# Kernel optimization log

Measured on AMD Instinct MI355X. Metric: run time of the kernel, lower is better.

## Reference

```python
import jax, jax.numpy as jnp
import numpy as np
from jax import lax

B, T, IN, H, OUT = 64, 512, 256, 1024, 512

def _uniform(key, shape, std):
    return jax.random.uniform(key, shape, jnp.float32, -std, std)

def setup_inputs() -> dict:
    key = jax.random.key(0)
    ks = jax.random.split(key, 12)
    std = 1.0 / np.sqrt(H)
    return {
        "x": jax.random.normal(ks[0], (B, T, IN), jnp.float32),
        "Wx0": _uniform(ks[1], (H, IN), std), "bx0": _uniform(ks[2], (H,), std),
        "Wh0": _uniform(ks[3], (H, H), std),  "bh0": _uniform(ks[4], (H,), std),
        "Wx1": _uniform(ks[5], (H, H), std),  "bx1": _uniform(ks[6], (H,), std),
        "Wh1": _uniform(ks[7], (H, H), std),  "bh1": _uniform(ks[8], (H,), std),
        "Wfc": _uniform(ks[9], (OUT, H), 1.0 / np.sqrt(H)),
        "bfc": _uniform(ks[10], (OUT,), 1.0 / np.sqrt(H)),
    }

def _run_layer(xs, Wx, bx, Wh, bh):
    # xs: [B, T, D_in] -> hidden sequence [B, T, H]
    xproj = jnp.einsum('btd,hd->bth', xs, Wx) + bx + bh  # precompute input projection
    def step(h, xp):
        h = jnp.tanh(xp + h @ Wh.T)
        return h, h
    h0 = jnp.zeros((xs.shape[0], Wh.shape[0]), xs.dtype)
    _, hs = lax.scan(step, h0, jnp.swapaxes(xproj, 0, 1))  # [T, B, H]
    return jnp.swapaxes(hs, 0, 1)

def reference(x, Wx0, bx0, Wh0, bh0, Wx1, bx1, Wh1, bh1, Wfc, bfc):
    h1 = _run_layer(x, Wx0, bx0, Wh0, bh0)   # layer 0 hidden sequence
    h2 = _run_layer(h1, Wx1, bx1, Wh1, bh1)  # layer 1 hidden sequence
    last = h2[:, -1, :]                       # last timestep of top layer
    return last @ Wfc.T + bfc
```

## Files before the change

### kernel.cpp

```cpp
#include <hip/hip_runtime.h>
#include <hip/hip_bf16.h>

#define Bb   64
#define Tt   512
#define INN  256
#define HH   1024
#define OUTN 512

#define NCOL 32
#define MG   16
#define NGRP (Bb / MG)
#define NSLOT 64
#define FSTR 8

typedef __attribute__((ext_vector_type(8))) short bf16x8;
typedef __attribute__((ext_vector_type(4))) float f32x4;

__device__ __forceinline__ unsigned short f2b(float f) {
  unsigned u = __float_as_uint(f);
  u += 0x7FFFu + ((u >> 16) & 1u);
  return (unsigned short)(u >> 16);
}
__device__ __forceinline__ float b2f(unsigned short u) {
  return __uint_as_float((unsigned)u << 16);
}

__device__ __forceinline__ unsigned int cohLoadU32(const unsigned int* p) {
  return __hip_atomic_load(p, __ATOMIC_RELAXED, __HIP_MEMORY_SCOPE_AGENT);
}
__device__ __forceinline__ unsigned long long cohLoadU64(const unsigned long long* p) {
  return __hip_atomic_load(p, __ATOMIC_RELAXED, __HIP_MEMORY_SCOPE_AGENT);
}
__device__ __forceinline__ unsigned short cohLoadU16(const unsigned short* p) {
  return __hip_atomic_load(p, __ATOMIC_RELAXED, __HIP_MEMORY_SCOPE_AGENT);
}
__device__ __forceinline__ void cohStoreU16(unsigned short* p, unsigned short v) {
  __hip_atomic_store(p, v, __ATOMIC_RELAXED, __HIP_MEMORY_SCOPE_AGENT);
}
__device__ __forceinline__ void cohStoreU32(unsigned int* p, unsigned int v) {
  __hip_atomic_store(p, v, __ATOMIC_RELAXED, __HIP_MEMORY_SCOPE_AGENT);
}

__device__ __forceinline__ void aload(bf16x8& d, const short* p) {
  asm volatile("global_load_dwordx4 %0, %1, off sc0 sc1" : "=v"(d) : "v"(p));
}
#define VMW(N)                                                   \
  do {                                                           \
    asm volatile("s_waitcnt vmcnt(" #N ")" ::: "memory");        \
    __builtin_amdgcn_sched_barrier(0);                           \
  } while (0)

__device__ __forceinline__ f32x4 splat4(float v) { f32x4 r = {v, v, v, v}; return r; }

union U16 { unsigned long long u[2]; bf16x8 v; };

__global__ void cvt4(const float* __restrict__ in, unsigned short* __restrict__ out, int n4) {
  int i = blockIdx.x * blockDim.x + threadIdx.x;
  if (i >= n4) return;
  float4 v = ((const float4*)in)[i];
  ushort4 o;
  o.x = f2b(v.x); o.y = f2b(v.y); o.z = f2b(v.z); o.w = f2b(v.w);
  ((ushort4*)out)[i] = o;
}

__global__ void addv(const float* __restrict__ a, const float* __restrict__ b,
                     float* __restrict__ o, int n) {
  int i = blockIdx.x * blockDim.x + threadIdx.x;
  if (i < n) o[i] = a[i] + b[i];
}

__global__ void zerok(unsigned int* __restrict__ p, int n) {
  int i = blockIdx.x * blockDim.x + threadIdx.x;
  if (i < n) p[i] = 0u;
}

__device__ __forceinline__ void waitflags(const unsigned int* gf, int l, unsigned need) {
#pragma clang loop unroll(disable)
  for (int guard = 0; guard < 4000000; ++guard) {
    unsigned f = cohLoadU32(gf + l * FSTR);
    if (__all((int)(f >= need))) return;
  }
}

__device__ __forceinline__ f32x4 comp8(const bf16x8* ab, const short* Wrow,
                                       int rx, int lh, int kk0, f32x4 acc) {
#pragma unroll
  for (int i = 0; i < 8; ++i) {
    const int s = (((kk0 + i) << 2) + lh) ^ rx;
    bf16x8 w = *(const bf16x8*)(Wrow + (s << 3));
    acc = __builtin_amdgcn_mfma_f32_16x16x32_bf16(ab[i], w, acc, 0, 0, 0);
  }
  return acc;
}

__device__ __forceinline__ f32x4 kphase(const short* Ap, const short* Wrow,
                                        int rx, int lh, f32x4 acc) {
  f32x4 acc2 = {0, 0, 0, 0};
  bf16x8 a0[8], a1[8];
#pragma unroll
  for (int i = 0; i < 8; ++i) aload(a0[i], Ap + i * 32);
#pragma unroll
  for (int i = 0; i < 8; ++i) aload(a1[i], Ap + 256 + i * 32);
  VMW(8);
  acc = comp8(a0, Wrow, rx, lh, 0, acc);
#pragma unroll
  for (int i = 0; i < 8; ++i) aload(a0[i], Ap + 512 + i * 32);
  VMW(8);
  acc2 = comp8(a1, Wrow, rx, lh, 8, acc2);
#pragma unroll
  for (int i = 0; i < 8; ++i) aload(a1[i], Ap + 768 + i * 32);
  VMW(8);
  acc = comp8(a0, Wrow, rx, lh, 16, acc);
  VMW(0);
  acc2 = comp8(a1, Wrow, rx, lh, 24, acc2);
  return acc + acc2;
}

__global__ __launch_bounds__(128) void rnn3(
    const __hip_bfloat16* __restrict__ xs,
    const __hip_bfloat16* __restrict__ Wx0, const __hip_bfloat16* __restrict__ Wh0,
    const __hip_bfloat16* __restrict__ Wx1, const __hip_bfloat16* __restrict__ Wh1,
    const float* __restrict__ b0s, const float* __restrict__ b1s,
    __hip_bfloat16* __restrict__ P0, __hip_bfloat16* __restrict__ P1,
    unsigned int* flags)
{
  __shared__ short Wl[NCOL * HH];
  const int tid = threadIdx.x;
  const int l   = tid & 63;
  const int wv  = tid >> 6;
  const int bid = blockIdx.x;
  const int stage = bid % 3;
  const int idx = bid / 3;
  const int j   = idx & 31;
  const int g   = idx >> 5;
  const int n0  = j * NCOL;
  const int rowA = g * MG;
  const int fr = l & 15;
  const int lh = l >> 4;
  const int rb = lh << 2;
  const int ccol = n0 + wv * 16 + fr;
  const int rx = (wv * 16 + fr) & 7;

  const short* Wg = (const short*)(stage == 0 ? Wh0 : (stage == 1 ? Wx1 : Wh1));
  for (int i = tid; i < NCOL * 128; i += 128) {
    const int r = i >> 7, p = i & 127, gs = p ^ (r & 7);
    *(bf16x8*)(Wl + r * HH + p * 8) = *(const bf16x8*)(Wg + (long)(n0 + r) * HH + gs * 8);
  }
  __syncthreads();
  const short* Wrow = Wl + (wv * 16 + fr) * HH;

  unsigned int* gf0 = flags + (0 * NGRP + g) * (NSLOT * FSTR);
  unsigned int* gfx = flags + (1 * NGRP + g) * (NSLOT * FSTR);
  unsigned int* gf1 = flags + (2 * NGRP + g) * (NSLOT * FSTR);
  const int wslot = (j * 2 + wv) * FSTR;
  const long laneA = (long)(rowA + fr) * HH + (lh << 3);
  unsigned short* P0u = (unsigned short*)P0;
  unsigned short* P1u = (unsigned short*)P1;

  if (stage == 0) {
    const float bias = b0s[ccol];
    const short* xrow = (const short*)xs + (long)(rowA + fr) * (Tt * INN) + (lh << 3);
    const short* Wx0row = (const short*)Wx0 + (long)ccol * INN + (lh << 3);
    bf16x8 wx[8];
#pragma unroll
    for (int c = 0; c < 8; ++c) wx[c] = *(const bf16x8*)(Wx0row + c * 32);
    f32x4 acc = splat4(bias);
#pragma unroll
    for (int c = 0; c < 8; ++c) {
      bf16x8 a = *(const bf16x8*)(xrow + c * 32);
      acc = __builtin_amdgcn_mfma_f32_16x16x32_bf16(a, wx[c], acc, 0, 0, 0);
    }
    for (int t = 0; t < Tt; ++t) {
      if (t > 0) {
        waitflags(gf0, l, (unsigned)t);
        acc = kphase((const short*)P0 + (long)(t - 1) * (Bb * HH) + laneA, Wrow, rx, lh, acc);
      }
      const long cb = ((long)t * Bb + rowA + rb) * HH + ccol;
#pragma unroll
      for (int r = 0; r < 4; ++r) cohStoreU16(P0u + cb + (long)r * HH, f2b(tanhf(acc[r])));
      asm volatile("s_waitcnt vmcnt(0)" ::: "memory");
      if (l == 0) cohStoreU32(gf0 + wslot, (unsigned)(t + 1));
      if (t + 1 < Tt) {
        acc = splat4(bias);
        const short* xr = xrow + (t + 1) * INN;
#pragma unroll
        for (int c = 0; c < 8; ++c) {
          bf16x8 a = *(const bf16x8*)(xr + c * 32);
          acc = __builtin_amdgcn_mfma_f32_16x16x32_bf16(a, wx[c], acc, 0, 0, 0);
        }
      }
    }
  } else if (stage == 1) {
    const float bias = b1s[ccol];
    for (int t = 0; t < Tt; ++t) {
      waitflags(gf0, l, (unsigned)(t + 1));
      f32x4 acc = kphase((const short*)P0 + (long)t * (Bb * HH) + laneA, Wrow, rx, lh,
                         splat4(bias));
      const long cb = ((long)t * Bb + rowA + rb) * HH + ccol;
#pragma unroll
      for (int r = 0; r < 4; ++r) cohStoreU16(P1u + cb + (long)r * HH, f2b(acc[r]));
      asm volatile("s_waitcnt vmcnt(0)" ::: "memory");
      if (l == 0) cohStoreU32(gfx + wslot, (unsigned)(t + 1));
    }
  } else {
    for (int t = 0; t < Tt; ++t) {
      waitflags(gfx, l, (unsigned)(t + 1));
      const long cb = ((long)t * Bb + rowA + rb) * HH + ccol;
      float xb[4];
#pragma unroll
      for (int r = 0; r < 4; ++r)
        xb[r] = b2f(cohLoadU16(P1u + cb + (long)r * HH));
      f32x4 acc = {0, 0, 0, 0};
      if (t > 0) {
        waitflags(gf1, l, (unsigned)t);
        acc = kphase((const short*)P1 + (long)(t - 1) * (Bb * HH) + laneA, Wrow, rx, lh, acc);
      }
#pragma unroll
      for (int r = 0; r < 4; ++r)
        cohStoreU16(P1u + cb + (long)r * HH, f2b(tanhf(acc[r] + xb[r])));
      asm volatile("s_waitcnt vmcnt(0)" ::: "memory");
      if (l == 0) cohStoreU32(gf1 + wslot, (unsigned)(t + 1));
    }
  }
}

__global__ void fc_kernel(const __hip_bfloat16* __restrict__ A,
                          const __hip_bfloat16* __restrict__ W,
                          const float* __restrict__ bias,
                          float* __restrict__ C)
{
  const int l   = threadIdx.x;
  const int m0  = blockIdx.x << 4;
  const int n0  = blockIdx.y << 6;
  const int r16 = l & 15;
  const int lh  = l >> 4;

  const unsigned long long* Au =
      (const unsigned long long*)((const short*)A + (long)(m0 + r16) * HH);
  const short* Wp = (const short*)W;
  const long w0 = (long)(n0 + r16) * HH + (lh << 3);
  const long wS = (long)HH << 4;

  f32x4 acc0 = {0,0,0,0}, acc1 = {0,0,0,0}, acc2 = {0,0,0,0}, acc3 = {0,0,0,0};
  for (int kc = 0; kc < HH; kc += 32) {
    U16 a;
    a.u[0] = cohLoadU64(Au + (kc >> 2) + (lh << 1));
    a.u[1] = cohLoadU64(Au + (kc >> 2) + (lh << 1) + 1);
    bf16x8 b0 = *(const bf16x8*)(Wp + w0 +          kc);
    bf16x8 b1 = *(const bf16x8*)(Wp + w0 + wS     + kc);
    bf16x8 b2 = *(const bf16x8*)(Wp + w0 + 2 * wS + kc);
    bf16x8 b3 = *(const bf16x8*)(Wp + w0 + 3 * wS + kc);
    acc0 = __builtin_amdgcn_mfma_f32_16x16x32_bf16(a.v, b0, acc0, 0, 0, 0);
    acc1 = __builtin_amdgcn_mfma_f32_16x16x32_bf16(a.v, b1, acc1, 0, 0, 0);
    acc2 = __builtin_amdgcn_mfma_f32_16x16x32_bf16(a.v, b2, acc2, 0, 0, 0);
    acc3 = __builtin_amdgcn_mfma_f32_16x16x32_bf16(a.v, b3, acc3, 0, 0, 0);
  }
  const int col = l & 15;
  const int rbb = (l >> 4) << 2;
#define FCEP(FIDX, ACC)                                                       \
  { const int n = n0 + (FIDX << 4) + col;                                     \
    _Pragma("unroll")                                                         \
    for (int r = 0; r < 4; ++r)                                               \
      C[(long)(m0 + rbb + r) * OUTN + n] = ACC[r] + bias[n]; }
  FCEP(0, acc0) FCEP(1, acc1) FCEP(2, acc2) FCEP(3, acc3)
#undef FCEP
}

extern "C" void kernel_launch(void* const* d_in, const int* in_sizes, int n_in,
                              void* d_out, int out_size, void* d_ws, size_t ws_size,
                              hipStream_t stream)
{
  const float* x   = (const float*)d_in[0];
  const float* Wx0 = (const float*)d_in[1];
  const float* bx0 = (const float*)d_in[2];
  const float* Wh0 = (const float*)d_in[3];
  const float* bh0 = (const float*)d_in[4];
  const float* Wx1 = (const float*)d_in[5];
  const float* bx1 = (const float*)d_in[6];
  const float* Wh1 = (const float*)d_in[7];
  const float* bh1 = (const float*)d_in[8];
  const float* Wfc = (const float*)d_in[9];
  const float* bfc = (const float*)d_in[10];

  char* ws = (char*)d_ws;
  const long SZ_XBF = (long)Bb * Tt * INN * 2;
  const long SZ_P   = (long)Bb * Tt * HH  * 2;
  __hip_bfloat16* xbf   = (__hip_bfloat16*)(ws);
  __hip_bfloat16* P0    = (__hip_bfloat16*)(ws + SZ_XBF);
  __hip_bfloat16* P1    = (__hip_bfloat16*)(ws + SZ_XBF + SZ_P);
  __hip_bfloat16* Wx0b  = (__hip_bfloat16*)(ws + SZ_XBF + 2 * SZ_P);
  __hip_bfloat16* Wh0b  = (__hip_bfloat16*)((char*)Wx0b + (long)HH * INN * 2);
  __hip_bfloat16* Wx1b  = (__hip_bfloat16*)((char*)Wh0b + (long)HH * HH * 2);
  __hip_bfloat16* Wh1b  = (__hip_bfloat16*)((char*)Wx1b + (long)HH * HH * 2);
  __hip_bfloat16* Wfcb  = (__hip_bfloat16*)((char*)Wh1b + (long)HH * HH * 2);
  float*          b0sum = (float*)((char*)Wfcb + (long)OUTN * HH * 2);
  float*          b1sum = (float*)((char*)b0sum + HH * 4);
  unsigned int*   flg   = (unsigned int*)((char*)b1sum + HH * 4);

  const int FLGN = 3 * NGRP * NSLOT * FSTR;

  {
    int n4;
    n4 = (Bb * Tt * INN) / 4; cvt4<<<(n4 + 255) / 256, 256, 0, stream>>>(x,   (unsigned short*)xbf,  n4);
    n4 = (HH * INN) / 4;      cvt4<<<(n4 + 255) / 256, 256, 0, stream>>>(Wx0, (unsigned short*)Wx0b, n4);
    n4 = (HH * HH) / 4;       cvt4<<<(n4 + 255) / 256, 256, 0, stream>>>(Wh0, (unsigned short*)Wh0b, n4);
    n4 = (HH * HH) / 4;       cvt4<<<(n4 + 255) / 256, 256, 0, stream>>>(Wx1, (unsigned short*)Wx1b, n4);
    n4 = (HH * HH) / 4;       cvt4<<<(n4 + 255) / 256, 256, 0, stream>>>(Wh1, (unsigned short*)Wh1b, n4);
    n4 = (OUTN * HH) / 4;     cvt4<<<(n4 + 255) / 256, 256, 0, stream>>>(Wfc, (unsigned short*)Wfcb, n4);
    addv<<<4, 256, 0, stream>>>(bx0, bh0, b0sum, HH);
    addv<<<4, 256, 0, stream>>>(bx1, bh1, b1sum, HH);
    zerok<<<(FLGN + 255) / 256, 256, 0, stream>>>(flg, FLGN);
  }

  rnn3<<<dim3(384), 128, 0, stream>>>(
      xbf, Wx0b, Wh0b, Wx1b, Wh1b, b0sum, b1sum, P0, P1, flg);

  fc_kernel<<<dim3(Bb / 16, OUTN / 64), 64, 0, stream>>>(
      P1 + (long)(Tt - 1) * Bb * HH, Wfcb, bfc, (float*)d_out);
}
```

Measured before the change: 3.604 ms.

## Hold recurrent weights in registers with 512-thread blocks and fewer flag slots

The weight slice moves out of LDS into VGPRs: each of 8 waves holds 32 bf16x8 fragments for its 16 columns, so there is no shared-memory read per MFMA. Blocks grow to 512 threads covering 128 columns, which cuts the grid to 96 blocks and the flag slots per group from 64 to 8. Flag publishing now goes through a __syncthreads per step, and the A-operand loads are rescheduled into a finer 4-deep pipeline with immediate offsets. Stage 2 now runs its recurrent matmul before waiting on the input-projection flag, which overlaps that wait with compute. The risks are heavy register pressure and fewer CUs in use.

```diff
diff --git a/kernel.cpp b/kernel.cpp
--- a/kernel.cpp
+++ b/kernel.cpp
@@ -7,11 +7,10 @@
 #define HH   1024
 #define OUTN 512
 
-#define NCOL 32
-#define MG   16
-#define NGRP (Bb / MG)
-#define NSLOT 64
-#define FSTR 8
+#define MG    16
+#define NGRP  (Bb / MG)
+#define NBLK2 8
+#define FSTR  8
 
 typedef __attribute__((ext_vector_type(8))) short bf16x8;
 typedef __attribute__((ext_vector_type(4))) float f32x4;
@@ -41,18 +40,18 @@
   __hip_atomic_store(p, v, __ATOMIC_RELAXED, __HIP_MEMORY_SCOPE_AGENT);
 }
 
-__device__ __forceinline__ void aload(bf16x8& d, const short* p) {
-  asm volatile("global_load_dwordx4 %0, %1, off sc0 sc1" : "=v"(d) : "v"(p));
-}
-#define VMW(N)                                                   \
-  do {                                                           \
-    asm volatile("s_waitcnt vmcnt(" #N ")" ::: "memory");        \
-    __builtin_amdgcn_sched_barrier(0);                           \
+__device__ __forceinline__ f32x4 splat4(float v) { f32x4 r = {v, v, v, v}; return r; }
+
+union U16 { unsigned long long u[2]; bf16x8 v; };
+
+#define ALOADO(d, p, OFF)                                                     \
+  asm volatile("global_load_dwordx4 %0, %1, off offset:" #OFF " sc0 sc1"      \
+               : "=v"(d) : "v"(p))
+#define VMW(N)                                                                \
+  do {                                                                        \
+    asm volatile("s_waitcnt vmcnt(" #N ")" ::: "memory");                     \
+    __builtin_amdgcn_sched_barrier(0);                                        \
   } while (0)
-
-__device__ __forceinline__ f32x4 splat4(float v) { f32x4 r = {v, v, v, v}; return r; }
-
-union U16 { unsigned long long u[2]; bf16x8 v; };
 
 __global__ void cvt4(const float* __restrict__ in, unsigned short* __restrict__ out, int n4) {
   int i = blockIdx.x * blockDim.x + threadIdx.x;
@@ -76,47 +75,38 @@
 
 __device__ __forceinline__ void waitflags(const unsigned int* gf, int l, unsigned need) {
 #pragma clang loop unroll(disable)
-  for (int guard = 0; guard < 4000000; ++guard) {
-    unsigned f = cohLoadU32(gf + l * FSTR);
+  for (int guard = 0; guard < 1000000; ++guard) {
+    unsigned f = cohLoadU32(gf + (l & 7) * FSTR);
     if (__all((int)(f >= need))) return;
   }
 }
 
-__device__ __forceinline__ f32x4 comp8(const bf16x8* ab, const short* Wrow,
-                                       int rx, int lh, int kk0, f32x4 acc) {
-#pragma unroll
-  for (int i = 0; i < 8; ++i) {
-    const int s = (((kk0 + i) << 2) + lh) ^ rx;
-    bf16x8 w = *(const bf16x8*)(Wrow + (s << 3));
-    acc = __builtin_amdgcn_mfma_f32_16x16x32_bf16(ab[i], w, acc, 0, 0, 0);
-  }
-  return acc;
-}
-
-__device__ __forceinline__ f32x4 kphase(const short* Ap, const short* Wrow,
-                                        int rx, int lh, f32x4 acc) {
+#define ISSUE4(B, O0, O1, O2, O3)                                             \
+  ALOADO(B##0, Ap, O0); ALOADO(B##1, Ap, O1);                                 \
+  ALOADO(B##2, Ap, O2); ALOADO(B##3, Ap, O3);
+#define COMP4(B, WI, ACC)                                                     \
+  ACC = __builtin_amdgcn_mfma_f32_16x16x32_bf16(B##0, w[(WI)],     ACC, 0,0,0);\
+  ACC = __builtin_amdgcn_mfma_f32_16x16x32_bf16(B##1, w[(WI) + 1], ACC, 0,0,0);\
+  ACC = __builtin_amdgcn_mfma_f32_16x16x32_bf16(B##2, w[(WI) + 2], ACC, 0,0,0);\
+  ACC = __builtin_amdgcn_mfma_f32_16x16x32_bf16(B##3, w[(WI) + 3], ACC, 0,0,0);
+
+__device__ __forceinline__ f32x4 kphase_reg(const short* Ap, const bf16x8* w, f32x4 acc) {
   f32x4 acc2 = {0, 0, 0, 0};
-  bf16x8 a0[8], a1[8];
-#pragma unroll
-  for (int i = 0; i < 8; ++i) aload(a0[i], Ap + i * 32);
-#pragma unroll
-  for (int i = 0; i < 8; ++i) aload(a1[i], Ap + 256 + i * 32);
-  VMW(8);
-  acc = comp8(a0, Wrow, rx, lh, 0, acc);
-#pragma unroll
-  for (int i = 0; i < 8; ++i) aload(a0[i], Ap + 512 + i * 32);
-  VMW(8);
-  acc2 = comp8(a1, Wrow, rx, lh, 8, acc2);
-#pragma unroll
-  for (int i = 0; i < 8; ++i) aload(a1[i], Ap + 768 + i * 32);
-  VMW(8);
-  acc = comp8(a0, Wrow, rx, lh, 16, acc);
-  VMW(0);
-  acc2 = comp8(a1, Wrow, rx, lh, 24, acc2);
+  bf16x8 a0_0, a0_1, a0_2, a0_3, a1_0, a1_1, a1_2, a1_3;
+  ISSUE4(a0_,    0,   64,  128,  192)
+  ISSUE4(a1_,  256,  320,  384,  448)
+  VMW(4); COMP4(a0_,  0, acc)  ISSUE4(a0_,  512,  576,  640,  704)
+  VMW(4); COMP4(a1_,  4, acc2) ISSUE4(a1_,  768,  832,  896,  960)
+  VMW(4); COMP4(a0_,  8, acc)  ISSUE4(a0_, 1024, 1088, 1152, 1216)
+  VMW(4); COMP4(a1_, 12, acc2) ISSUE4(a1_, 1280, 1344, 1408, 1472)
+  VMW(4); COMP4(a0_, 16, acc)  ISSUE4(a0_, 1536, 1600, 1664, 1728)
+  VMW(4); COMP4(a1_, 20, acc2) ISSUE4(a1_, 1792, 1856, 1920, 1984)
+  VMW(4); COMP4(a0_, 24, acc)
+  VMW(0); COMP4(a1_, 28, acc2)
   return acc + acc2;
 }
 
-__global__ __launch_bounds__(128) void rnn3(
+__global__ __launch_bounds__(512, 2) void rnn3r(
     const __hip_bfloat16* __restrict__ xs,
     const __hip_bfloat16* __restrict__ Wx0, const __hip_bfloat16* __restrict__ Wh0,
     const __hip_bfloat16* __restrict__ Wx1, const __hip_bfloat16* __restrict__ Wh1,
@@ -124,38 +114,33 @@
     __hip_bfloat16* __restrict__ P0, __hip_bfloat16* __restrict__ P1,
     unsigned int* flags)
 {
-  __shared__ short Wl[NCOL * HH];
   const int tid = threadIdx.x;
   const int l   = tid & 63;
   const int wv  = tid >> 6;
   const int bid = blockIdx.x;
   const int stage = bid % 3;
   const int idx = bid / 3;
-  const int j   = idx & 31;
-  const int g   = idx >> 5;
-  const int n0  = j * NCOL;
+  const int j   = idx & 7;
+  const int g   = idx >> 3;
   const int rowA = g * MG;
   const int fr = l & 15;
   const int lh = l >> 4;
   const int rb = lh << 2;
-  const int ccol = n0 + wv * 16 + fr;
-  const int rx = (wv * 16 + fr) & 7;
-
-  const short* Wg = (const short*)(stage == 0 ? Wh0 : (stage == 1 ? Wx1 : Wh1));
-  for (int i = tid; i < NCOL * 128; i += 128) {
-    const int r = i >> 7, p = i & 127, gs = p ^ (r & 7);
-    *(bf16x8*)(Wl + r * HH + p * 8) = *(const bf16x8*)(Wg + (long)(n0 + r) * HH + gs * 8);
-  }
-  __syncthreads();
-  const short* Wrow = Wl + (wv * 16 + fr) * HH;
-
-  unsigned int* gf0 = flags + (0 * NGRP + g) * (NSLOT * FSTR);
-  unsigned int* gfx = flags + (1 * NGRP + g) * (NSLOT * FSTR);
-  unsigned int* gf1 = flags + (2 * NGRP + g) * (NSLOT * FSTR);
-  const int wslot = (j * 2 + wv) * FSTR;
+  const int ccol = j * 128 + wv * 16 + fr;
+
+  unsigned int* gf0 = flags + (0 * NGRP + g) * (NBLK2 * FSTR);
+  unsigned int* gfx = flags + (1 * NGRP + g) * (NBLK2 * FSTR);
+  unsigned int* gf1 = flags + (2 * NGRP + g) * (NBLK2 * FSTR);
+  const int wslot = j * FSTR;
   const long laneA = (long)(rowA + fr) * HH + (lh << 3);
   unsigned short* P0u = (unsigned short*)P0;
   unsigned short* P1u = (unsigned short*)P1;
+
+  const short* Wg = (const short*)(stage == 0 ? Wh0 : (stage == 1 ? Wx1 : Wh1));
+  const short* Wgrow = Wg + (long)ccol * HH + (lh << 3);
+  bf16x8 w[32];
+#pragma unroll
+  for (int c = 0; c < 32; ++c) w[c] = *(const bf16x8*)(Wgrow + (c << 5));
 
   if (stage == 0) {
     const float bias = b0s[ccol];
@@ -163,29 +148,31 @@
     const short* Wx0row = (const short*)Wx0 + (long)ccol * INN + (lh << 3);
     bf16x8 wx[8];
 #pragma unroll
-    for (int c = 0; c < 8; ++c) wx[c] = *(const bf16x8*)(Wx0row + c * 32);
+    for (int c = 0; c < 8; ++c) wx[c] = *(const bf16x8*)(Wx0row + (c << 5));
     f32x4 acc = splat4(bias);
 #pragma unroll
     for (int c = 0; c < 8; ++c) {
-      bf16x8 a = *(const bf16x8*)(xrow + c * 32);
+      bf16x8 a = *(const bf16x8*)(xrow + (c << 5));
       acc = __builtin_amdgcn_mfma_f32_16x16x32_bf16(a, wx[c], acc, 0, 0, 0);
     }
     for (int t = 0; t < Tt; ++t) {
       if (t > 0) {
         waitflags(gf0, l, (unsigned)t);
-        acc = kphase((const short*)P0 + (long)(t - 1) * (Bb * HH) + laneA, Wrow, rx, lh, acc);
+        acc = kphase_reg((const short*)P0 + (long)(t - 1) * (Bb * HH) + laneA, w, acc);
       }
       const long cb = ((long)t * Bb + rowA + rb) * HH + ccol;
 #pragma unroll
-      for (int r = 0; r < 4; ++r) cohStoreU16(P0u + cb + (long)r * HH, f2b(tanhf(acc[r])));
+      for (int r = 0; r < 4; ++r)
+        cohStoreU16(P0u + cb + (long)r * HH, f2b(tanhf(acc[r])));
       asm volatile("s_waitcnt vmcnt(0)" ::: "memory");
-      if (l == 0) cohStoreU32(gf0 + wslot, (unsigned)(t + 1));
+      __syncthreads();
+      if (tid == 0) cohStoreU32(gf0 + wslot, (unsigned)(t + 1));
       if (t + 1 < Tt) {
         acc = splat4(bias);
         const short* xr = xrow + (t + 1) * INN;
 #pragma unroll
         for (int c = 0; c < 8; ++c) {
-          bf16x8 a = *(const bf16x8*)(xr + c * 32);
+          bf16x8 a = *(const bf16x8*)(xr + (c << 5));
           acc = __builtin_amdgcn_mfma_f32_16x16x32_bf16(a, wx[c], acc, 0, 0, 0);
         }
       }
@@ -194,32 +181,35 @@
     const float bias = b1s[ccol];
     for (int t = 0; t < Tt; ++t) {
       waitflags(gf0, l, (unsigned)(t + 1));
-      f32x4 acc = kphase((const short*)P0 + (long)t * (Bb * HH) + laneA, Wrow, rx, lh,
-                         splat4(bias));
+      f32x4 acc = kphase_reg((const short*)P0 + (long)t * (Bb * HH) + laneA, w,
+                             splat4(bias));
       const long cb = ((long)t * Bb + rowA + rb) * HH + ccol;
 #pragma unroll
-      for (int r = 0; r < 4; ++r) cohStoreU16(P1u + cb + (long)r * HH, f2b(acc[r]));
+      for (int r = 0; r < 4; ++r)
+        cohStoreU16(P1u + cb + (long)r * HH, f2b(acc[r]));
       asm volatile("s_waitcnt vmcnt(0)" ::: "memory");
-      if (l == 0) cohStoreU32(gfx + wslot, (unsigned)(t + 1));
+      __syncthreads();
+      if (tid == 0) cohStoreU32(gfx + wslot, (unsigned)(t + 1));
     }
   } else {
     for (int t = 0; t < Tt; ++t) {
+      f32x4 acc = {0, 0, 0, 0};
+      if (t > 0) {
+        waitflags(gf1, l, (unsigned)t);
+        acc = kphase_reg((const short*)P1 + (long)(t - 1) * (Bb * HH) + laneA, w, acc);
+      }
       waitflags(gfx, l, (unsigned)(t + 1));
       const long cb = ((long)t * Bb + rowA + rb) * HH + ccol;
       float xb[4];
 #pragma unroll
       for (int r = 0; r < 4; ++r)
         xb[r] = b2f(cohLoadU16(P1u + cb + (long)r * HH));
-      f32x4 acc = {0, 0, 0, 0};
-      if (t > 0) {
-        waitflags(gf1, l, (unsigned)t);
-        acc = kphase((const short*)P1 + (long)(t - 1) * (Bb * HH) + laneA, Wrow, rx, lh, acc);
-      }
 #pragma unroll
       for (int r = 0; r < 4; ++r)
         cohStoreU16(P1u + cb + (long)r * HH, f2b(tanhf(acc[r] + xb[r])));
       asm volatile("s_waitcnt vmcnt(0)" ::: "memory");
-      if (l == 0) cohStoreU32(gf1 + wslot, (unsigned)(t + 1));
+      __syncthreads();
+      if (tid == 0) cohStoreU32(gf1 + wslot, (unsigned)(t + 1));
     }
   }
 }
@@ -297,7 +287,7 @@
   float*          b1sum = (float*)((char*)b0sum + HH * 4);
   unsigned int*   flg   = (unsigned int*)((char*)b1sum + HH * 4);
 
-  const int FLGN = 3 * NGRP * NSLOT * FSTR;
+  const int FLGN = 3 * NGRP * NBLK2 * FSTR;
 
   {
     int n4;
@@ -312,7 +302,7 @@
     zerok<<<(FLGN + 255) / 256, 256, 0, stream>>>(flg, FLGN);
   }
 
-  rnn3<<<dim3(384), 128, 0, stream>>>(
+  rnn3r<<<dim3(3 * NGRP * NBLK2), 512, 0, stream>>>(
       xbf, Wx0b, Wh0b, Wx1b, Wh1b, b0sum, b1sum, P0, P1, flg);
 
   fc_kernel<<<dim3(Bb / 16, OUTN / 64), 64, 0, stream>>>(
```

New measurement: 5.317 ms. 1.48x slower.
